# Optimization experiments

Hardware: AMD Instinct MI355X
Metric: run time of the kernel (lower is better)

## Reference

```python
import jax, jax.numpy as jnp
import numpy as np

EPS = 1e-6
HID = 2048; N_HEADS = 16; Q_LORA = 768; KV_LORA = 512
ROPE_D = 64; NOPE_D = 128; V_D = 128
IDX_H = 32; IDX_D = 128; IDX_TOPK = 512
N_EXP = 8; TOPK = 4; N_GROUP = 4; TOPK_GROUP = 2
MOE_I = 512; SHARED_I = 512; ROUTED_SCALE = 2.5
T = 1024
NEG = -1e30


def _rms(x, w, eps=EPS):
    x = x.astype(jnp.float32)
    return x * jax.lax.rsqrt(jnp.mean(x * x, axis=-1, keepdims=True) + eps) * w


def _ln(x, w, b, eps=EPS):
    x = x.astype(jnp.float32)
    m = jnp.mean(x, axis=-1, keepdims=True)
    v = jnp.mean((x - m) ** 2, axis=-1, keepdims=True)
    return (x - m) * jax.lax.rsqrt(v + eps) * w + b


def _rope_cs(positions, dim):
    inv = 1.0 / (10000.0 ** (jnp.arange(0, dim, 2, dtype=jnp.float32) / dim))
    f = positions.astype(jnp.float32)[:, None] * inv[None, :]  # [T, dim/2]
    return jnp.cos(f), jnp.sin(f)


def _rope(x, cos, sin):
    # neox-style rotate-half over last dim
    d = x.shape[-1] // 2
    x1, x2 = x[..., :d], x[..., d:]
    while cos.ndim < x.ndim:
        cos, sin = cos[:, None], sin[:, None]
    return jnp.concatenate([x1 * cos - x2 * sin, x2 * cos + x1 * sin], axis=-1)


def setup_inputs() -> dict:
    key = jax.random.key(0)
    ks = iter(jax.random.split(key, 32))
    w = lambda *s: jax.random.normal(next(ks), s, jnp.float32) * 0.02
    inp = {
        'positions': jnp.arange(T, dtype=jnp.int32),
        'hidden_states': jax.random.normal(next(ks), (T, HID), jnp.float32),
        'residual': jax.random.normal(next(ks), (T, HID), jnp.float32),
        'w_input_ln': jnp.ones((HID,), jnp.float32),
        'w_post_ln': jnp.ones((HID,), jnp.float32),
        'w_step1': w(Q_LORA + KV_LORA + ROPE_D + IDX_D + IDX_H, HID),
        'w_q_a_ln': jnp.ones((Q_LORA,), jnp.float32),
        'w_kv_a_ln': jnp.ones((KV_LORA,), jnp.float32),
        'idx_k_ln_w': jnp.ones((IDX_D,), jnp.float32),
        'idx_k_ln_b': jnp.zeros((IDX_D,), jnp.float32),
        'w_step3': w(IDX_H * IDX_D + N_HEADS * (NOPE_D + ROPE_D), Q_LORA),
        'W_UK_T': w(N_HEADS, NOPE_D, KV_LORA),
        'W_UV': w(N_HEADS, KV_LORA, V_D),
        'w_o': w(HID, N_HEADS * V_D),
        'gate_w': w(N_EXP, HID),
        'gate_bias': jnp.zeros((N_EXP,), jnp.float32),
        'shared_gate_up': w(2 * SHARED_I, HID),
        'shared_down': w(HID, SHARED_I),
        'exp_gate_up': w(N_EXP, 2 * MOE_I, HID),
        'exp_down': w(N_EXP, HID, MOE_I),
    }
    return inp


def reference(positions, hidden_states, residual, w_input_ln, w_post_ln, w_step1,
              w_q_a_ln, w_kv_a_ln, idx_k_ln_w, idx_k_ln_b, w_step3, W_UK_T, W_UV,
              w_o, gate_w, gate_bias, shared_gate_up, shared_down, exp_gate_up, exp_down):
    Tn = hidden_states.shape[0]
    rows = jnp.arange(Tn)
    # (allreduce is identity at tp=1) + residual add + RMSNorm
    res = hidden_states.astype(jnp.float32) + residual.astype(jnp.float32)
    h = _rms(res, w_input_ln)
    # ---- Step 1: fused qkv_a + indexer_wk + indexer_weights_proj GEMM ----
    s1 = h @ w_step1.T
    o0 = 0
    q_c = s1[:, o0:o0 + Q_LORA]; o0 += Q_LORA
    kv_c = s1[:, o0:o0 + KV_LORA]; o0 += KV_LORA
    k_pe = s1[:, o0:o0 + ROPE_D]; o0 += ROPE_D
    idx_k = s1[:, o0:o0 + IDX_D]; o0 += IDX_D
    idx_w_raw = s1[:, o0:o0 + IDX_H]
    cos, sin = _rope_cs(positions, ROPE_D)
    # fused_norm_rope: norms + rope on k_pe / indexer-k
    q_c = _rms(q_c, w_q_a_ln)
    kv_c = _rms(kv_c, w_kv_a_ln)
    k_pe = _rope(k_pe, cos, sin)
    idx_k = _ln(idx_k, idx_k_ln_w, idx_k_ln_b)
    idx_k = jnp.concatenate([_rope(idx_k[:, :ROPE_D], cos, sin), idx_k[:, ROPE_D:]], axis=-1)
    # ---- Step 3: fused indexer_wq_b + q_b_proj GEMM ----
    s3 = q_c @ w_step3.T
    idx_q = s3[:, :IDX_H * IDX_D].reshape(Tn, IDX_H, IDX_D)
    q = s3[:, IDX_H * IDX_D:].reshape(Tn, N_HEADS, NOPE_D + ROPE_D)
    q_nope, q_pe = q[..., :NOPE_D], q[..., NOPE_D:]
    # absorb W_UK: [T,H,nope] x [H,nope,kv_lora] -> [T,H,kv_lora]
    ql_nope = jnp.einsum('thn,hnk->thk', q_nope, W_UK_T)
    q_pe = _rope(q_pe, cos, sin)
    idx_q = jnp.concatenate([_rope(idx_q[..., :ROPE_D], cos, sin), idx_q[..., ROPE_D:]], axis=-1)
    idx_q = idx_q * (IDX_D ** -0.5)            # indexer softmax scale
    idx_w = idx_w_raw * (IDX_H ** -0.5)        # per-head weights scale
    # ---- sparse attention indexer: relu(q.k) head-weighted sum, causal top-k ----
    il = jnp.einsum('thd,sd->ths', idx_q, idx_k)          # [T,Hi,S]
    iscores = jnp.einsum('ths,th->ts', jax.nn.relu(il), idx_w)
    causal = positions[:, None] >= positions[None, :]
    iscores = jnp.where(causal, iscores, NEG)
    topk_idx = jax.lax.top_k(iscores, IDX_TOPK)[1]        # [T, IDX_TOPK]
    tmask = jnp.zeros((Tn, Tn), bool).at[rows[:, None], topk_idx].set(True)
    mask = causal & tmask
    # ---- MLA MQA attention in latent space ----
    mqa_q = jnp.concatenate([ql_nope, jnp.broadcast_to(q_pe, (Tn, N_HEADS, ROPE_D))], axis=-1)
    kv = jnp.concatenate([kv_c, k_pe], axis=-1)           # [S, kv_lora+rope]
    att = jnp.einsum('thd,sd->hts', mqa_q, kv) * ((NOPE_D + ROPE_D) ** -0.5)
    att = jnp.where(mask[None], att, NEG)
    p = jax.nn.softmax(att, axis=-1)
    o = jnp.einsum('hts,sk->thk', p, kv_c)                # [T,H,kv_lora]
    o = jnp.einsum('thk,hkv->thv', o, W_UV).reshape(Tn, N_HEADS * V_D)
    attn_out = o @ w_o.T
    # add + RMSNorm
    res2 = attn_out + res
    h2 = _rms(res2, w_post_ln)
    # ---- MoE: DeepSeekV3 sigmoid grouped routing + shared experts ----
    glog = h2 @ gate_w.T
    sg = jax.nn.sigmoid(glog)
    sc = sg + gate_bias
    gsz = N_EXP // N_GROUP
    grp = sc.reshape(Tn, N_GROUP, gsz)
    grp_score = jax.lax.top_k(grp, min(2, gsz))[0].sum(-1)
    gidx = jax.lax.top_k(grp_score, TOPK_GROUP)[1]
    gmask = jnp.zeros((Tn, N_GROUP), bool).at[rows[:, None], gidx].set(True)
    emask = jnp.repeat(gmask, gsz, axis=1)
    sc_m = jnp.where(emask, sc, NEG)
    _, tid = jax.lax.top_k(sc_m, TOPK)
    tw = jnp.take_along_axis(sg, tid, axis=1)
    tw = tw / (tw.sum(-1, keepdims=True) + 1e-20) * ROUTED_SCALE
    comb = jnp.zeros((Tn, N_EXP), jnp.float32).at[rows[:, None], tid].set(tw)
    # routed experts (dense masked combine as reference for grouped-GEMM dispatch)
    gu = jnp.einsum('th,eih->tei', h2, exp_gate_up)       # [T,E,2I]
    act = jax.nn.silu(gu[..., :MOE_I]) * gu[..., MOE_I:]
    routed_e = jnp.einsum('tei,ehi->teh', act, exp_down)  # [T,E,H]
    routed = jnp.einsum('te,teh->th', comb, routed_e)
    # shared experts
    gus = h2 @ shared_gate_up.T
    shared = (jax.nn.silu(gus[:, :SHARED_I]) * gus[:, SHARED_I:]) @ shared_down.T
    out = shared + routed
    return out, res2
```

## Files before the change

kernel.cpp:

```cpp
#include <hip/hip_runtime.h>
#include <math.h>

static constexpr int TT  = 1024;
static constexpr int HID = 2048;
static constexpr int NH  = 16;
static constexpr int QL  = 768;
static constexpr int KVL = 512;
static constexpr int RD  = 64;
static constexpr int IH  = 32;
static constexpr int ID  = 128;
static constexpr int S1W = QL + KVL + RD + ID + IH;
static constexpr int S3W = IH*ID + NH*(128+RD);

#define SCALE_ATT 0.07216878364870323f
#define SC_IDXQ   0.08838834764831845f
#define SC_IDXW   0.17677669529663687f
#define NEGR      -1e30f
#define NEGL      -3.0e38f

typedef __bf16 bf16x8 __attribute__((ext_vector_type(8)));
typedef float  f32x4  __attribute__((ext_vector_type(4)));

#define GLD_LDS16(g, l) __builtin_amdgcn_global_load_lds( \
    (const __attribute__((address_space(1))) void*)(g),   \
    (__attribute__((address_space(3))) void*)(l), 16, 0, 0)

__device__ __forceinline__ unsigned short f2b(float x) {
  union { float f; unsigned u; } v; v.f = x;
  unsigned r = v.u + 0x7FFFu + ((v.u >> 16) & 1u);
  return (unsigned short)(r >> 16);
}
__device__ __forceinline__ float b2f(unsigned short u) {
  union { unsigned u; float f; } v; v.u = ((unsigned)u) << 16;
  return v.f;
}

__device__ __forceinline__ float blk_sum256(float v, float* s) {
  #pragma unroll
  for (int o = 32; o > 0; o >>= 1) v += __shfl_down(v, o, 64);
  __syncthreads();
  if ((threadIdx.x & 63) == 0) s[threadIdx.x >> 6] = v;
  __syncthreads();
  return s[0] + s[1] + s[2] + s[3];
}

__global__ __launch_bounds__(256) void k_prelude(const float* __restrict__ hs,
                                                 const float* __restrict__ rsd,
                                                 const float* __restrict__ w,
                                                 float* __restrict__ res,
                                                 unsigned short* __restrict__ hb) {
  int t = blockIdx.x;
  __shared__ float scr[4];
  float vals[8]; float ss = 0.f;
  #pragma unroll
  for (int r = 0; r < 8; r++) {
    int d = threadIdx.x + 256*r;
    float v = hs[(size_t)t*HID + d] + rsd[(size_t)t*HID + d];
    vals[r] = v; res[(size_t)t*HID + d] = v; ss = fmaf(v, v, ss);
  }
  ss = blk_sum256(ss, scr);
  float inv = 1.f/sqrtf(ss/(float)HID + 1e-6f);
  #pragma unroll
  for (int r = 0; r < 8; r++) {
    int d = threadIdx.x + 256*r;
    hb[(size_t)t*HID + d] = f2b(vals[r]*inv*w[d]);
  }
}

__global__ __launch_bounds__(256) void k_res2(const float* __restrict__ attn1,
                                              const float* __restrict__ attn2,
                                              const float* __restrict__ res,
                                              const float* __restrict__ w,
                                              float* __restrict__ res2_out,
                                              float* __restrict__ h2,
                                              unsigned short* __restrict__ h2b) {
  int t = blockIdx.x;
  __shared__ float scr[4];
  float vals[8]; float ss = 0.f;
  #pragma unroll
  for (int r = 0; r < 8; r++) {
    int d = threadIdx.x + 256*r;
    float v = attn1[(size_t)t*HID + d] + attn2[(size_t)t*HID + d] + res[(size_t)t*HID + d];
    vals[r] = v; res2_out[(size_t)t*HID + d] = v; ss = fmaf(v, v, ss);
  }
  ss = blk_sum256(ss, scr);
  float inv = 1.f/sqrtf(ss/(float)HID + 1e-6f);
  #pragma unroll
  for (int r = 0; r < 8; r++) {
    int d = threadIdx.x + 256*r;
    float o = vals[r]*inv*w[d];
    h2[(size_t)t*HID + d] = o;
    h2b[(size_t)t*HID + d] = f2b(o);
  }
}

__global__ void k_ropecs(const int* __restrict__ pos, float* __restrict__ cosb, float* __restrict__ sinb) {
  int i = blockIdx.x*256 + threadIdx.x;
  if (i >= TT*32) return;
  int t = i >> 5, k = i & 31;
  double inv = pow(10000.0, -((double)(2*k))/64.0);
  double f = (double)pos[t] * inv;
  cosb[i] = (float)cos(f);
  sinb[i] = (float)sin(f);
}

__global__ void k_f2b(const float* __restrict__ s, unsigned short* __restrict__ d,
                      long long n, long long ntot) {
  long long stride = (long long)gridDim.x * 1024;
  for (long long i = ((long long)blockIdx.x*256 + threadIdx.x)*4; i < ntot; i += stride) {
    float x0, x1, x2, x3;
    if (i + 3 < n) { float4 v = *(const float4*)(s + i); x0=v.x; x1=v.y; x2=v.z; x3=v.w; }
    else {
      x0 = (i   < n) ? s[i]   : 0.f; x1 = (i+1 < n) ? s[i+1] : 0.f;
      x2 = (i+2 < n) ? s[i+2] : 0.f; x3 = (i+3 < n) ? s[i+3] : 0.f;
    }
    ushort4 o; o.x=f2b(x0); o.y=f2b(x1); o.z=f2b(x2); o.w=f2b(x3);
    *(ushort4*)(d + i) = o;
  }
}

__global__ void k_f2b4(const float* __restrict__ s0, unsigned short* __restrict__ d0, long long n0,
                       const float* __restrict__ s1, unsigned short* __restrict__ d1, long long n1,
                       const float* __restrict__ s2, unsigned short* __restrict__ d2, long long n2,
                       const float* __restrict__ s3, unsigned short* __restrict__ d3, long long n3) {
  long long ntot = n0 + n1 + n2 + n3;
  long long stride = (long long)gridDim.x * 1024;
  for (long long i = ((long long)blockIdx.x*256 + threadIdx.x)*4; i < ntot; i += stride) {
    const float* s; unsigned short* d; long long j = i;
    if (j < n0) { s = s0; d = d0; }
    else { j -= n0;
      if (j < n1) { s = s1; d = d1; }
      else { j -= n1;
        if (j < n2) { s = s2; d = d2; }
        else { j -= n2; s = s3; d = d3; } } }
    float4 v = *(const float4*)(s + j);
    ushort4 o; o.x=f2b(v.x); o.y=f2b(v.y); o.z=f2b(v.z); o.w=f2b(v.w);
    *(ushort4*)(d + j) = o;
  }
}

__global__ __launch_bounds__(256) void k_tconvb(const float* __restrict__ src,
                                                unsigned short* __restrict__ dst,
                                                int R, int C) {
  src += (size_t)blockIdx.z * R * C;
  dst += (size_t)blockIdx.z * R * C;
  __shared__ float tile[32][33];
  int c0 = blockIdx.x * 32, r0 = blockIdx.y * 32;
  int tx = threadIdx.x & 31, ty = threadIdx.x >> 5;
  #pragma unroll
  for (int i = 0; i < 4; i++) {
    int r = r0 + ty + i*8;
    tile[ty + i*8][tx] = src[(size_t)r*C + c0 + tx];
  }
  __syncthreads();
  #pragma unroll
  for (int i = 0; i < 4; i++) {
    int c = c0 + ty + i*8;
    dst[(size_t)c*R + r0 + tx] = f2b(tile[tx][ty + i*8]);
  }
}

template<int OUT, bool ILV>
__global__ __launch_bounds__(256) void k_mgemm(
    const unsigned short* __restrict__ A, int lda, long long sA,
    const unsigned short* __restrict__ B, int ldb, long long sB,
    void* __restrict__ Cv, int ldc, long long sC,
    int N, int K, float alpha, int cskip, int ktri,
    int nseg, long long segA, long long segB,
    const float* __restrict__ comb) {
  const int row0 = blockIdx.y * 128;
  const int col0 = blockIdx.x * 128;
  if (cskip >= 0 && col0 > row0 + cskip) return;
  __shared__ __align__(16) unsigned short As[128*64];
  __shared__ __align__(16) unsigned short Bs[128*64];
  const int tid  = threadIdx.x;
  const int wave = tid >> 6, lane = tid & 63;
  const int wm = wave >> 1, wn = wave & 1;
  const int zb = blockIdx.z;
  A += (size_t)zb * (size_t)sA;
  B += (size_t)zb * (size_t)sB;

  f32x4 acc[4][4] = {};
  const int l15 = lane & 15, l4 = lane >> 4;
  const int sx = l15 & 7;
  const int Kend = (ktri && K > row0 + 128) ? (row0 + 128) : K;

  for (int seg = 0; seg < nseg; seg++) {
    const unsigned short* Ab = A + (size_t)seg * segA;
    const unsigned short* Bb = B + (size_t)seg * segB;
    for (int k0 = 0; k0 < Kend; k0 += 64) {
      __syncthreads();
      #pragma unroll
      for (int it = 0; it < 4; it++) {
        int base = wave*64 + it*256;
        int sidx = base + lane;
        int r = sidx >> 3, s = sidx & 7;
        int s_src = s ^ (r & 7);
        const unsigned short* ga = Ab + (size_t)(row0 + r)*lda + k0 + s_src*8;
        GLD_LDS16(ga, As + base*8);
        int rt = col0 + r;
        int srow = ILV ? ((rt >> 1) + (rt & 1)*512) : rt;
        const unsigned short* gb = Bb + (size_t)srow*ldb + k0 + s_src*8;
        GLD_LDS16(gb, Bs + base*8);
      }
      __syncthreads();
      #pragma unroll
      for (int kc = 0; kc < 2; kc++) {
        const int sl = ((kc*4 + l4) ^ sx) << 3;
        bf16x8 fa[4], fb[4];
        #pragma unroll
        for (int mf = 0; mf < 4; mf++)
          fa[mf] = *(const bf16x8*)&As[(wm*64 + mf*16 + l15)*64 + sl];
        #pragma unroll
        for (int nf = 0; nf < 4; nf++)
          fb[nf] = *(const bf16x8*)&Bs[(wn*64 + nf*16 + l15)*64 + sl];
        #pragma unroll
        for (int mf = 0; mf < 4; mf++)
          #pragma unroll
          for (int nf = 0; nf < 4; nf++)
            acc[mf][nf] = __builtin_amdgcn_mfma_f32_16x16x32_bf16(fa[mf], fb[nf], acc[mf][nf], 0, 0, 0);
      }
    }
  }

  #pragma unroll
  for (int mf = 0; mf < 4; mf++) {
    #pragma unroll
    for (int nf = 0; nf < 4; nf++) {
      int n = col0 + wn*64 + nf*16 + l15;
      #pragma unroll
      for (int r = 0; r < 4; r++) {
        int m = row0 + wm*64 + mf*16 + l4*4 + r;
        float v = acc[mf][nf][r] * alpha;
        if (OUT == 2) {
          float p = __shfl_xor(v, 1, 64);
          if ((l15 & 1) == 0) {
            float w = (zb < 8) ? comb[m*8 + zb] : 1.f;
            float rres = v/(1.f + expf(-v)) * p * w;
            ((unsigned short*)Cv)[(size_t)zb*sC + (size_t)m*ldc + (n >> 1)] = f2b(rres);
          }
        } else if (n < N) {
          size_t idx = (size_t)m*ldc + n;
          if (OUT == 1) ((unsigned short*)Cv)[(size_t)zb*sC + idx] = f2b(v);
          else          ((float*)Cv)[(size_t)zb*sC + idx] = v;
        }
      }
    }
  }
}

__global__ __launch_bounds__(256) void k_post1(const float* __restrict__ s1a,
    const float* __restrict__ s1b,
    const float* __restrict__ wq, const float* __restrict__ wkv,
    const float* __restrict__ lnw, const float* __restrict__ lnb,
    const float* __restrict__ cosb, const float* __restrict__ sinb,
    unsigned short* __restrict__ qcb, float* __restrict__ kvc, float* __restrict__ kpe,
    float* __restrict__ idxk, float* __restrict__ idxw) {
  int t = blockIdx.x, tid = threadIdx.x;
  __shared__ float rowb[S1W];
  __shared__ float scr[4];
  __shared__ float yb[128];
  for (int d = tid; d < S1W; d += 256)
    rowb[d] = s1a[(size_t)t*S1W + d] + s1b[(size_t)t*S1W + d];
  __syncthreads();
  float ss = 0.f;
  for (int d = tid; d < QL; d += 256) { float v = rowb[d]; ss = fmaf(v,v,ss); }
  ss = blk_sum256(ss, scr);
  float inv = 1.f/sqrtf(ss/(float)QL + 1e-6f);
  for (int d = tid; d < QL; d += 256) qcb[(size_t)t*QL + d] = f2b(rowb[d]*inv*wq[d]);
  ss = 0.f;
  for (int d = tid; d < KVL; d += 256) { float v = rowb[QL+d]; ss = fmaf(v,v,ss); }
  ss = blk_sum256(ss, scr);
  inv = 1.f/sqrtf(ss/(float)KVL + 1e-6f);
  for (int d = tid; d < KVL; d += 256) kvc[(size_t)t*KVL + d] = rowb[QL+d]*inv*wkv[d];
  float sm = (tid < 128) ? rowb[1344 + tid] : 0.f;
  float tot = blk_sum256(sm, scr);
  float mean = tot / 128.f;
  float vs = 0.f;
  if (tid < 128) { float v = rowb[1344+tid] - mean; vs = v*v; }
  vs = blk_sum256(vs, scr);
  float ivn = 1.f/sqrtf(vs/128.f + 1e-6f);
  if (tid < 128) yb[tid] = (rowb[1344+tid]-mean)*ivn*lnw[tid] + lnb[tid];
  __syncthreads();
  if (tid < 32) {
    float c = cosb[t*32 + tid], s = sinb[t*32 + tid];
    idxk[(size_t)t*ID + tid]      = yb[tid]*c - yb[32+tid]*s;
    idxk[(size_t)t*ID + 32 + tid] = yb[32+tid]*c + yb[tid]*s;
    float x1 = rowb[1280+tid], x2 = rowb[1312+tid];
    kpe[(size_t)t*RD + tid]      = x1*c - x2*s;
    kpe[(size_t)t*RD + 32 + tid] = x2*c + x1*s;
    idxw[(size_t)t*IH + tid] = rowb[1472+tid] * SC_IDXW;
  } else if (tid >= 64 && tid < 128) {
    idxk[(size_t)t*ID + tid] = yb[tid];
  }
}

__global__ __launch_bounds__(256) void k_post3b(const float* __restrict__ s3,
                                                const float* __restrict__ cosb,
                                                const float* __restrict__ sinb,
                                                unsigned short* __restrict__ s3b) {
  int t = blockIdx.x, tid = threadIdx.x;
  const float* row = s3 + (size_t)t*S3W;
  __shared__ float buf[S3W];
  __shared__ float cs[32], sn[32];
  if (tid < 32) { cs[tid] = cosb[t*32+tid]; sn[tid] = sinb[t*32+tid]; }
  for (int d = tid; d < S3W; d += 256) buf[d] = row[d];
  __syncthreads();
  for (int p = tid; p < 1024; p += 256) {
    int h = p >> 5, d = p & 31;
    float c = cs[d], s = sn[d];
    float x1 = buf[h*ID + d], x2 = buf[h*ID + 32 + d];
    buf[h*ID + d]      = (x1*c - x2*s) * SC_IDXQ;
    buf[h*ID + 32 + d] = (x2*c + x1*s) * SC_IDXQ;
  }
  for (int p = tid; p < 2048; p += 256) {
    int h = p >> 6, d = 64 + (p & 63);
    buf[h*ID + d] *= SC_IDXQ;
  }
  for (int p = tid; p < 512; p += 256) {
    int h = p >> 5, d = p & 31;
    float c = cs[d], s = sn[d];
    int base = IH*ID + h*192 + 128;
    float x1 = buf[base + d], x2 = buf[base + 32 + d];
    buf[base + d]      = x1*c - x2*s;
    buf[base + 32 + d] = x2*c + x1*s;
  }
  __syncthreads();
  unsigned short* orow = s3b + (size_t)t*S3W;
  for (int g = tid*4; g < S3W; g += 1024) {
    ushort4 o;
    o.x = f2b(buf[g]); o.y = f2b(buf[g+1]); o.z = f2b(buf[g+2]); o.w = f2b(buf[g+3]);
    *(ushort4*)(orow + g) = o;
  }
}

__global__ void k_qpe(const unsigned short* __restrict__ s3b, unsigned short* __restrict__ qm) {
  int i = blockIdx.x*256 + threadIdx.x;
  int t = i >> 10, r = i & 1023;
  int h = r >> 6, j = r & 63;
  float v = b2f(s3b[(size_t)t*S3W + IH*ID + h*192 + 128 + j]) * SCALE_ATT;
  qm[(size_t)t*9216 + h*576 + 512 + j] = f2b(v);
}

__global__ void k_kvb(const float* __restrict__ kvc, const float* __restrict__ kpe,
                      unsigned short* __restrict__ kvb) {
  int i = blockIdx.x*256 + threadIdx.x;
  int s = i / 576, d = i - s*576;
  float v = (d < 512) ? kvc[(size_t)s*KVL + d] : kpe[(size_t)s*RD + (d - 512)];
  kvb[i] = f2b(v);
}

__global__ __launch_bounds__(256) void k_ired(const float* __restrict__ il,
                                              const float* __restrict__ idxw,
                                              float* __restrict__ isc,
                                              int first, int last, int h0) {
  int tr = blockIdx.x;
  int t = 512 + tr;
  int s0 = threadIdx.x * 4;
  float4 acc;
  if (first) acc = make_float4(0.f, 0.f, 0.f, 0.f);
  else       acc = *(float4*)(isc + (size_t)tr*TT + s0);
  #pragma unroll
  for (int hh = 0; hh < 8; hh++) {
    float w = idxw[t*IH + h0 + hh];
    float4 v = *(const float4*)(il + (size_t)hh*524288 + (size_t)tr*1024 + s0);
    acc.x += fmaxf(v.x, 0.f) * w;
    acc.y += fmaxf(v.y, 0.f) * w;
    acc.z += fmaxf(v.z, 0.f) * w;
    acc.w += fmaxf(v.w, 0.f) * w;
  }
  if (last) {
    if (s0     > t) acc.x = NEGR;
    if (s0 + 1 > t) acc.y = NEGR;
    if (s0 + 2 > t) acc.z = NEGR;
    if (s0 + 3 > t) acc.w = NEGR;
  }
  *(float4*)(isc + (size_t)tr*TT + s0) = acc;
}

__global__ __launch_bounds__(512) void k_topk(const float* __restrict__ isc,
                                              unsigned char* __restrict__ mask) {
  int t = 512 + blockIdx.x;
  const float* row = isc + (size_t)blockIdx.x * TT;
  __shared__ unsigned long long keys[1024];
  int tid = threadIdx.x;
  for (int i = tid; i < 1024; i += 512) {
    float v = row[i];
    unsigned int b = __float_as_uint(v);
    unsigned int u = (b & 0x80000000u) ? ~b : (b | 0x80000000u);
    keys[i] = ((unsigned long long)u << 32) | (unsigned int)(1023 - i);
  }
  __syncthreads();
  for (int k = 2; k <= 1024; k <<= 1) {
    for (int j = k >> 1; j > 0; j >>= 1) {
      int i = ((tid & ~(j - 1)) << 1) | (tid & (j - 1));
      int l = i | j;
      unsigned long long a = keys[i], b = keys[l];
      bool up = ((i & k) == 0);
      if ((a < b) == up) { keys[i] = b; keys[l] = a; }
      __syncthreads();
    }
  }
  unsigned char* mrow = mask + (size_t)t * TT;
  for (int p = tid; p < 1024; p += 512) {
    int s = 1023 - (int)(keys[p] & 0xFFFFFFFFu);
    mrow[s] = (p < 512) ? (unsigned char)1 : (unsigned char)0;
  }
}

__global__ __launch_bounds__(256) void k_psoft(unsigned short* __restrict__ pb,
                                               const unsigned char* __restrict__ mask) {
  int b = blockIdx.x;
  int t = b & 1023, h = b >> 10;
  unsigned short* row = pb + ((size_t)h << 20) + ((size_t)t << 10);
  int tid = threadIdx.x;
  __shared__ float scr[4];
  int s0 = tid * 4;
  int rub = ((t >> 7) + 1) << 7;
  bool act = (s0 < rub);
  float v0 = 0.f, v1 = 0.f, v2 = 0.f, v3 = 0.f;
  bool m0 = false, m1 = false, m2 = false, m3 = false;
  if (act) {
    ushort4 raw = *(const ushort4*)(row + s0);
    v0 = b2f(raw.x); v1 = b2f(raw.y); v2 = b2f(raw.z); v3 = b2f(raw.w);
    if (t < 512) {
      m0 = (s0 <= t); m1 = (s0+1 <= t); m2 = (s0+2 <= t); m3 = (s0+3 <= t);
    } else {
      uchar4 mk = *(const uchar4*)(mask + (size_t)t*TT + s0);
      m0 = (s0 <= t) && mk.x; m1 = (s0+1 <= t) && mk.y;
      m2 = (s0+2 <= t) && mk.z; m3 = (s0+3 <= t) && mk.w;
    }
  }
  float mx = NEGL;
  if (m0) mx = v0;
  if (m1) mx = fmaxf(mx, v1);
  if (m2) mx = fmaxf(mx, v2);
  if (m3) mx = fmaxf(mx, v3);
  #pragma unroll
  for (int o = 32; o > 0; o >>= 1) mx = fmaxf(mx, __shfl_down(mx, o, 64));
  __syncthreads();
  if ((tid & 63) == 0) scr[tid >> 6] = mx;
  __syncthreads();
  mx = fmaxf(fmaxf(scr[0], scr[1]), fmaxf(scr[2], scr[3]));
  float p0 = m0 ? expf(v0 - mx) : 0.f;
  float p1 = m1 ? expf(v1 - mx) : 0.f;
  float p2 = m2 ? expf(v2 - mx) : 0.f;
  float p3 = m3 ? expf(v3 - mx) : 0.f;
  float sum = blk_sum256((p0+p1)+(p2+p3), scr);
  float inv = 1.f / sum;
  if (act) {
    ushort4 o;
    o.x = f2b(p0*inv); o.y = f2b(p1*inv); o.z = f2b(p2*inv); o.w = f2b(p3*inv);
    *(ushort4*)(row + s0) = o;
  }
}

__global__ __launch_bounds__(256) void k_gate(const float* __restrict__ h2,
                                              const float* __restrict__ gw,
                                              const float* __restrict__ gb,
                                              float* __restrict__ comb) {
  int t = blockIdx.x, tid = threadIdx.x;
  int e = tid >> 5, lane = tid & 31;
  __shared__ float gl[8];
  float p = 0.f;
  for (int d = lane; d < HID; d += 32) p = fmaf(h2[(size_t)t*HID+d], gw[(size_t)e*HID+d], p);
  #pragma unroll
  for (int o = 16; o > 0; o >>= 1) p += __shfl_down(p, o, 32);
  if (lane == 0) gl[e] = p;
  __syncthreads();
  if (tid == 0) {
    float sg[8], sc[8];
    #pragma unroll
    for (int i = 0; i < 8; i++) { sg[i] = 1.f/(1.f+expf(-gl[i])); sc[i] = sg[i] + gb[i]; }
    float gs[4];
    #pragma unroll
    for (int g = 0; g < 4; g++) gs[g] = sc[2*g] + sc[2*g+1];
    int g0 = 0;
    for (int g = 1; g < 4; g++) if (gs[g] > gs[g0]) g0 = g;
    int g1 = -1;
    for (int g = 0; g < 4; g++) { if (g == g0) continue; if (g1 < 0 || gs[g] > gs[g1]) g1 = g; }
    float wsum = 1e-20f;
    #pragma unroll
    for (int i = 0; i < 8; i++) { int g = i >> 1; if (g == g0 || g == g1) wsum += sg[i]; }
    #pragma unroll
    for (int i = 0; i < 8; i++) { int g = i >> 1; comb[t*8+i] = (g == g0 || g == g1) ? sg[i]/wsum*2.5f : 0.f; }
  }
}

__global__ void k_dnred(const float* __restrict__ r, float* __restrict__ o) {
  int i = (blockIdx.x*256 + threadIdx.x)*4;
  float4 a = *(const float4*)(r + i);
  float4 b = *(const float4*)(r + 2097152 + i);
  float4 c = *(const float4*)(r + 4194304 + i);
  float4 v;
  v.x = a.x + b.x + c.x; v.y = a.y + b.y + c.y;
  v.z = a.z + b.z + c.z; v.w = a.w + b.w + c.w;
  *(float4*)(o + i) = v;
}

extern "C" void kernel_launch(void* const* d_in, const int* in_sizes, int n_in,
                              void* d_out, int out_size, void* d_ws, size_t ws_size,
                              hipStream_t stream) {
  const int*   positions = (const int*)d_in[0];
  const float* hs     = (const float*)d_in[1];
  const float* rsd    = (const float*)d_in[2];
  const float* w_in   = (const float*)d_in[3];
  const float* w_post = (const float*)d_in[4];
  const float* w_s1   = (const float*)d_in[5];
  const float* w_qln  = (const float*)d_in[6];
  const float* w_kvln = (const float*)d_in[7];
  const float* iklnw  = (const float*)d_in[8];
  const float* iklnb  = (const float*)d_in[9];
  const float* w_s3   = (const float*)d_in[10];
  const float* wukt   = (const float*)d_in[11];
  const float* wuv    = (const float*)d_in[12];
  const float* w_o    = (const float*)d_in[13];
  const float* gate_w = (const float*)d_in[14];
  const float* gate_b = (const float*)d_in[15];
  const float* sh_gu  = (const float*)d_in[16];
  const float* sh_dn  = (const float*)d_in[17];
  const float* ex_gu  = (const float*)d_in[18];
  const float* ex_dn  = (const float*)d_in[19];

  float* ws = (float*)d_ws;
  typedef unsigned short ush;
  float* RES   = ws + 0;
  float* COSB  = ws + 2097152;
  float* SINB  = ws + 2129920;
  float* KVC   = ws + 2162688;
  float* KPE   = ws + 2686976;
  float* IDXK  = ws + 2752512;
  float* IDXW  = ws + 2883584;
  float* COMB  = ws + 2916352;
  ush*   HB    = (ush*)(ws + 2924544);
  ush*   WS1B  = (ush*)(ws + 3973120);
  float* S1P0  = ws + 5545984;
  ush*   QCB   = (ush*)(ws + 7086080);
  ush*   WS3B  = (ush*)(ws + 7479296);
  ush*   WOB   = (ush*)(ws + 7479296);
  float* S3    = ws + 10231808;
  float* S1P1  = ws + 10231808;
  ush*   S3B   = (ush*)(ws + 17571840);
  ush*   WUKTB = (ush*)(ws + 21241856);
  ush*   QMQAB = (ush*)(ws + 21766144);
  float* ISC   = ws + 26484736;
  unsigned char* MASK = (unsigned char*)(ws + 27009024);
  ush*   WUVB  = (ush*)(ws + 27271168);
  ush*   KVB   = (ush*)(ws + 27795456);
  ush*   VTB   = (ush*)(ws + 28090368);
  ush*   O2B   = (ush*)(ws + 28352512);
  float* ILB   = ws + 27795456;
  ush*   IDXKB = (ush*)(ws + 31989760);
  ush*   PB    = (ush*)(ws + 10231808);
  ush*   OHB   = (ush*)(ws + 18620416);
  float* ATTNP = ws + 10231808;
  float* H2     = ws + 2924544;
  ush*   H2B    = (ush*)(ws + 5021696);
  ush*   EXGUB  = (ush*)(ws + 6070272);
  ush*   SHGUB  = (ush*)(ws + 14458880);
  ush*   EXDNB  = (ush*)(ws + 15507456);
  ush*   SHDNB  = (ush*)(ws + 19701760);
  ush*   ACTB9  = (ush*)(ws + 20226048);
  float* RPART  = ws + 22585344;

  float* OUT0 = (float*)d_out;
  float* OUT_RES2 = OUT0 + (size_t)TT*HID;

  k_prelude<<<TT, 256, 0, stream>>>(hs, rsd, w_in, RES, HB);
  k_ropecs<<<(TT*32)/256, 256, 0, stream>>>(positions, COSB, SINB);
  k_f2b<<<1024, 256, 0, stream>>>(w_s1, WS1B, 3080192LL, 3145728LL);
  k_f2b<<<1024, 256, 0, stream>>>(w_s3, WS3B, 5505024LL, 5505024LL);
  k_tconvb<<<dim3(16,4,16), 256, 0, stream>>>(wukt, WUKTB, 128, 512);
  k_tconvb<<<dim3(4,16,16), 256, 0, stream>>>(wuv, WUVB, 512, 128);
  k_mgemm<0,false><<<dim3(12,8,2), 256, 0, stream>>>(
      HB, 2048, 1024, WS1B, 2048, 1024, S1P0, S1W, 4685824,
      1504, 1024, 1.f, -1, 0, 1, 0, 0, nullptr);
  k_post1<<<TT, 256, 0, stream>>>(S1P0, S1P1, w_qln, w_kvln, iklnw, iklnb, COSB, SINB, QCB, KVC, KPE, IDXK, IDXW);
  k_f2b<<<128, 256, 0, stream>>>(IDXK, IDXKB, 131072LL, 131072LL);
  k_mgemm<0,false><<<dim3(56,8,1), 256, 0, stream>>>(
      QCB, 768, 0, WS3B, 768, 0, S3, S3W, 0,
      S3W, 768, 1.f, -1, 0, 1, 0, 0, nullptr);
  k_post3b<<<TT, 256, 0, stream>>>(S3, COSB, SINB, (ush*)S3B);
  k_f2b<<<1024, 256, 0, stream>>>(w_o, WOB, 4194304LL, 4194304LL);
  k_mgemm<1,false><<<dim3(4,8,16), 256, 0, stream>>>(
      S3B + 4096, S3W, 192, WUKTB, 128, 65536, QMQAB, 9216, 576,
      512, 128, SCALE_ATT, -1, 0, 1, 0, 0, nullptr);
  k_qpe<<<4096, 256, 0, stream>>>(S3B, QMQAB);
  for (int c = 0; c < 4; c++) {
    k_mgemm<0,false><<<dim3(8,4,8), 256, 0, stream>>>(
        S3B + (size_t)512*S3W + c*1024, S3W, 128, IDXKB, 128, 0,
        ILB, 1024, 524288, 1024, 128, 1.f, 639, 0, 1, 0, 0, nullptr);
    k_ired<<<512, 256, 0, stream>>>(ILB, IDXW, ISC, c == 0, c == 3, c*8);
  }
  k_topk<<<512, 512, 0, stream>>>(ISC, MASK);
  k_kvb<<<2304, 256, 0, stream>>>(KVC, KPE, KVB);
  k_tconvb<<<dim3(16,32,1), 256, 0, stream>>>(KVC, VTB, 1024, 512);
  k_mgemm<1,false><<<dim3(8,8,16), 256, 0, stream>>>(
      QMQAB, 9216, 576, KVB, 576, 0, PB, 1024, 1048576,
      1024, 576, 1.f, 127, 0, 1, 0, 0, nullptr);
  k_psoft<<<16384, 256, 0, stream>>>(PB, MASK);
  k_mgemm<1,false><<<dim3(4,8,16), 256, 0, stream>>>(
      PB, 1024, 1048576, VTB, 1024, 0, OHB, 512, 524288,
      512, 1024, 1.f, -1, 1, 1, 0, 0, nullptr);
  k_mgemm<1,false><<<dim3(1,8,16), 256, 0, stream>>>(
      OHB, 512, 524288, WUVB, 512, 65536, O2B, 2048, 128,
      128, 512, 1.f, -1, 0, 1, 0, 0, nullptr);
  k_mgemm<0,false><<<dim3(16,8,2), 256, 0, stream>>>(
      O2B, 2048, 1024, WOB, 2048, 1024, ATTNP, 2048, 2097152,
      2048, 1024, 1.f, -1, 0, 1, 0, 0, nullptr);
  k_res2<<<TT, 256, 0, stream>>>(ATTNP, ATTNP + 2097152, RES, w_post, OUT_RES2, H2, H2B);
  k_gate<<<TT, 256, 0, stream>>>(H2, gate_w, gate_b, COMB);
  k_f2b4<<<2048, 256, 0, stream>>>(ex_gu, EXGUB, 16777216LL,
                                   sh_gu, SHGUB, 2097152LL,
                                   ex_dn, EXDNB, 8388608LL,
                                   sh_dn, SHDNB, 1048576LL);
  k_mgemm<2,true><<<dim3(8,8,9), 256, 0, stream>>>(
      H2B, 2048, 0, EXGUB, 2048, 2097152, ACTB9, 512, 524288,
      1024, 2048, 1.f, -1, 0, 1, 0, 0, COMB);
  k_mgemm<0,false><<<dim3(16,8,3), 256, 0, stream>>>(
      ACTB9, 512, 1572864, EXDNB, 512, 3145728, RPART, 2048, 2097152,
      2048, 512, 1.f, -1, 0, 3, 524288, 1048576, nullptr);
  k_dnred<<<2048, 256, 0, stream>>>(RPART, OUT0);
}
```

Before: 443.7 us.

## Replace dense masked MoE with routed grouped-GEMM token dispatch

```diff
diff --git a/kernel.cpp b/kernel.cpp
--- a/kernel.cpp
+++ b/kernel.cpp
@@ -160,25 +160,42 @@
   }
 }
 
-template<int OUT, bool ILV>
+template<int OUT, bool ILV, int MOE>
 __global__ __launch_bounds__(256) void k_mgemm(
     const unsigned short* __restrict__ A, int lda, long long sA,
     const unsigned short* __restrict__ B, int ldb, long long sB,
     void* __restrict__ Cv, int ldc, long long sC,
     int N, int K, float alpha, int cskip, int ktri,
     int nseg, long long segA, long long segB,
-    const float* __restrict__ comb) {
+    const float* __restrict__ comb,
+    const int* __restrict__ cntp, const int* __restrict__ tokp) {
   const int row0 = blockIdx.y * 128;
   const int col0 = blockIdx.x * 128;
   if (cskip >= 0 && col0 > row0 + cskip) return;
+  const int zb = blockIdx.z;
+  int cnt = 0; long long off = 0;
+  if (MOE) {
+    cnt = cntp[zb];
+    for (int e = 0; e < zb; e++) off += cntp[e];
+    if (row0 >= cnt) return;
+  }
   __shared__ __align__(16) unsigned short As[128*64];
   __shared__ __align__(16) unsigned short Bs[128*64];
   const int tid  = threadIdx.x;
   const int wave = tid >> 6, lane = tid & 63;
   const int wm = wave >> 1, wn = wave & 1;
-  const int zb = blockIdx.z;
   A += (size_t)zb * (size_t)sA;
   B += (size_t)zb * (size_t)sB;
+  if (MOE == 2) A += off * (long long)lda;
+
+  int tki[4];
+  if (MOE == 1) {
+    #pragma unroll
+    for (int it = 0; it < 4; it++) {
+      int r = (wave*64 + it*256 + lane) >> 3;
+      tki[it] = tokp[zb*1024 + row0 + r];
+    }
+  }
 
   f32x4 acc[4][4] = {};
   const int l15 = lane & 15, l4 = lane >> 4;
@@ -196,7 +213,9 @@
         int sidx = base + lane;
         int r = sidx >> 3, s = sidx & 7;
         int s_src = s ^ (r & 7);
-        const unsigned short* ga = Ab + (size_t)(row0 + r)*lda + k0 + s_src*8;
+        const unsigned short* ga;
+        if (MOE == 1) ga = Ab + (size_t)tki[it]*lda + k0 + s_src*8;
+        else          ga = Ab + (size_t)(row0 + r)*lda + k0 + s_src*8;
         GLD_LDS16(ga, As + base*8);
         int rt = col0 + r;
         int srow = ILV ? ((rt >> 1) + (rt & 1)*512) : rt;
@@ -235,14 +254,30 @@
         if (OUT == 2) {
           float p = __shfl_xor(v, 1, 64);
           if ((l15 & 1) == 0) {
-            float w = (zb < 8) ? comb[m*8 + zb] : 1.f;
-            float rres = v/(1.f + expf(-v)) * p * w;
-            ((unsigned short*)Cv)[(size_t)zb*sC + (size_t)m*ldc + (n >> 1)] = f2b(rres);
+            bool ok = true;
+            long long mrow = m;
+            float w;
+            if (MOE == 1) {
+              ok = (m < cnt); mrow = off + m;
+              int tok = tokp[zb*1024 + m];
+              w = (zb < 8) ? comb[tok*8 + zb] : 1.f;
+            } else {
+              w = (zb < 8) ? comb[m*8 + zb] : 1.f;
+            }
+            if (ok) {
+              float rres = v/(1.f + expf(-v)) * p * w;
+              ((unsigned short*)Cv)[(size_t)zb*sC + (size_t)mrow*ldc + (n >> 1)] = f2b(rres);
+            }
           }
         } else if (n < N) {
-          size_t idx = (size_t)m*ldc + n;
-          if (OUT == 1) ((unsigned short*)Cv)[(size_t)zb*sC + idx] = f2b(v);
-          else          ((float*)Cv)[(size_t)zb*sC + idx] = v;
+          bool ok = true;
+          long long mrow = m;
+          if (MOE == 2) { ok = (m < cnt); mrow = off + m; }
+          if (ok) {
+            size_t idx = (size_t)mrow*ldc + n;
+            if (OUT == 1) ((unsigned short*)Cv)[(size_t)zb*sC + idx] = f2b(v);
+            else          ((float*)Cv)[(size_t)zb*sC + idx] = v;
+          }
         }
       }
     }
@@ -487,15 +522,62 @@
   }
 }
 
-__global__ void k_dnred(const float* __restrict__ r, float* __restrict__ o) {
-  int i = (blockIdx.x*256 + threadIdx.x)*4;
-  float4 a = *(const float4*)(r + i);
-  float4 b = *(const float4*)(r + 2097152 + i);
-  float4 c = *(const float4*)(r + 4194304 + i);
-  float4 v;
-  v.x = a.x + b.x + c.x; v.y = a.y + b.y + c.y;
-  v.z = a.z + b.z + c.z; v.w = a.w + b.w + c.w;
-  *(float4*)(o + i) = v;
+__global__ __launch_bounds__(1024) void k_route(const float* __restrict__ comb,
+                                                int* __restrict__ tokidx,
+                                                int* __restrict__ rank,
+                                                int* __restrict__ cntp) {
+  int e = blockIdx.x;
+  int t = threadIdx.x;
+  if (e == 8) {
+    tokidx[8*1024 + t] = t;
+    if (t == 0) cntp[8] = 1024;
+    return;
+  }
+  int lane = t & 63, w = t >> 6;
+  bool sel = comb[t*8 + e] != 0.0f;
+  unsigned long long bal = __ballot(sel);
+  int pw = __popcll(bal & ((1ull << lane) - 1ull));
+  int wt = __popcll(bal);
+  __shared__ int wsum[16];
+  if (lane == 0) wsum[w] = wt;
+  __syncthreads();
+  int woff = 0, total = 0;
+  #pragma unroll
+  for (int i = 0; i < 16; i++) { int v = wsum[i]; if (i < w) woff += v; total += v; }
+  int pos = woff + pw;
+  rank[t*8 + e] = sel ? pos : -1;
+  if (sel) tokidx[e*1024 + pos] = t;
+  __syncthreads();
+  if (t >= total) tokidx[e*1024 + t] = 0;
+  if (t == 0) cntp[e] = total;
+}
+
+__global__ __launch_bounds__(256) void k_rsum(const float* __restrict__ dpc,
+                                              const int* __restrict__ rank,
+                                              const int* __restrict__ cntp,
+                                              float* __restrict__ out) {
+  int t = blockIdx.x;
+  int d = threadIdx.x * 8;
+  int offs[8]; int acc_off = 0;
+  #pragma unroll
+  for (int e = 0; e < 8; e++) { offs[e] = acc_off; acc_off += cntp[e]; }
+  const float* ps = dpc + (size_t)(acc_off + t)*2048 + d;
+  float4 a0 = *(const float4*)ps;
+  float4 a1 = *(const float4*)(ps + 4);
+  #pragma unroll
+  for (int e = 0; e < 8; e++) {
+    int r = rank[t*8 + e];
+    if (r >= 0) {
+      const float* p = dpc + (size_t)(offs[e] + r)*2048 + d;
+      float4 b0 = *(const float4*)p;
+      float4 b1 = *(const float4*)(p + 4);
+      a0.x += b0.x; a0.y += b0.y; a0.z += b0.z; a0.w += b0.w;
+      a1.x += b1.x; a1.y += b1.y; a1.z += b1.z; a1.w += b1.w;
+    }
+  }
+  float* po = out + (size_t)t*2048 + d;
+  *(float4*)po = a0;
+  *(float4*)(po + 4) = a1;
 }
 
 extern "C" void kernel_launch(void* const* d_in, const int* in_sizes, int n_in,
@@ -560,8 +642,11 @@
   ush*   SHGUB  = (ush*)(ws + 14458880);
   ush*   EXDNB  = (ush*)(ws + 15507456);
   ush*   SHDNB  = (ush*)(ws + 19701760);
-  ush*   ACTB9  = (ush*)(ws + 20226048);
-  float* RPART  = ws + 22585344;
+  ush*   ACTC   = (ush*)(ws + 20226048);
+  float* DPC    = ws + 21536768;
+  int*   TOKIDX = (int*)(ws + 32022528);
+  int*   RANK   = (int*)(ws + 32031744);
+  int*   CNT    = (int*)(ws + 32039936);
 
   float* OUT0 = (float*)d_out;
   float* OUT_RES2 = OUT0 + (size_t)TT*HID;
@@ -572,53 +657,54 @@
   k_f2b<<<1024, 256, 0, stream>>>(w_s3, WS3B, 5505024LL, 5505024LL);
   k_tconvb<<<dim3(16,4,16), 256, 0, stream>>>(wukt, WUKTB, 128, 512);
   k_tconvb<<<dim3(4,16,16), 256, 0, stream>>>(wuv, WUVB, 512, 128);
-  k_mgemm<0,false><<<dim3(12,8,2), 256, 0, stream>>>(
+  k_mgemm<0,false,0><<<dim3(12,8,2), 256, 0, stream>>>(
       HB, 2048, 1024, WS1B, 2048, 1024, S1P0, S1W, 4685824,
-      1504, 1024, 1.f, -1, 0, 1, 0, 0, nullptr);
+      1504, 1024, 1.f, -1, 0, 1, 0, 0, nullptr, nullptr, nullptr);
   k_post1<<<TT, 256, 0, stream>>>(S1P0, S1P1, w_qln, w_kvln, iklnw, iklnb, COSB, SINB, QCB, KVC, KPE, IDXK, IDXW);
   k_f2b<<<128, 256, 0, stream>>>(IDXK, IDXKB, 131072LL, 131072LL);
-  k_mgemm<0,false><<<dim3(56,8,1), 256, 0, stream>>>(
+  k_mgemm<0,false,0><<<dim3(56,8,1), 256, 0, stream>>>(
       QCB, 768, 0, WS3B, 768, 0, S3, S3W, 0,
-      S3W, 768, 1.f, -1, 0, 1, 0, 0, nullptr);
+      S3W, 768, 1.f, -1, 0, 1, 0, 0, nullptr, nullptr, nullptr);
   k_post3b<<<TT, 256, 0, stream>>>(S3, COSB, SINB, (ush*)S3B);
   k_f2b<<<1024, 256, 0, stream>>>(w_o, WOB, 4194304LL, 4194304LL);
-  k_mgemm<1,false><<<dim3(4,8,16), 256, 0, stream>>>(
+  k_mgemm<1,false,0><<<dim3(4,8,16), 256, 0, stream>>>(
       S3B + 4096, S3W, 192, WUKTB, 128, 65536, QMQAB, 9216, 576,
-      512, 128, SCALE_ATT, -1, 0, 1, 0, 0, nullptr);
+      512, 128, SCALE_ATT, -1, 0, 1, 0, 0, nullptr, nullptr, nullptr);
   k_qpe<<<4096, 256, 0, stream>>>(S3B, QMQAB);
   for (int c = 0; c < 4; c++) {
-    k_mgemm<0,false><<<dim3(8,4,8), 256, 0, stream>>>(
+    k_mgemm<0,false,0><<<dim3(8,4,8), 256, 0, stream>>>(
         S3B + (size_t)512*S3W + c*1024, S3W, 128, IDXKB, 128, 0,
-        ILB, 1024, 524288, 1024, 128, 1.f, 639, 0, 1, 0, 0, nullptr);
+        ILB, 1024, 524288, 1024, 128, 1.f, 639, 0, 1, 0, 0, nullptr, nullptr, nullptr);
     k_ired<<<512, 256, 0, stream>>>(ILB, IDXW, ISC, c == 0, c == 3, c*8);
   }
   k_topk<<<512, 512, 0, stream>>>(ISC, MASK);
   k_kvb<<<2304, 256, 0, stream>>>(KVC, KPE, KVB);
   k_tconvb<<<dim3(16,32,1), 256, 0, stream>>>(KVC, VTB, 1024, 512);
-  k_mgemm<1,false><<<dim3(8,8,16), 256, 0, stream>>>(
+  k_mgemm<1,false,0><<<dim3(8,8,16), 256, 0, stream>>>(
       QMQAB, 9216, 576, KVB, 576, 0, PB, 1024, 1048576,
-      1024, 576, 1.f, 127, 0, 1, 0, 0, nullptr);
+      1024, 576, 1.f, 127, 0, 1, 0, 0, nullptr, nullptr, nullptr);
   k_psoft<<<16384, 256, 0, stream>>>(PB, MASK);
-  k_mgemm<1,false><<<dim3(4,8,16), 256, 0, stream>>>(
+  k_mgemm<1,false,0><<<dim3(4,8,16), 256, 0, stream>>>(
       PB, 1024, 1048576, VTB, 1024, 0, OHB, 512, 524288,
-      512, 1024, 1.f, -1, 1, 1, 0, 0, nullptr);
-  k_mgemm<1,false><<<dim3(1,8,16), 256, 0, stream>>>(
+      512, 1024, 1.f, -1, 1, 1, 0, 0, nullptr, nullptr, nullptr);
+  k_mgemm<1,false,0><<<dim3(1,8,16), 256, 0, stream>>>(
       OHB, 512, 524288, WUVB, 512, 65536, O2B, 2048, 128,
-      128, 512, 1.f, -1, 0, 1, 0, 0, nullptr);
-  k_mgemm<0,false><<<dim3(16,8,2), 256, 0, stream>>>(
+      128, 512, 1.f, -1, 0, 1, 0, 0, nullptr, nullptr, nullptr);
+  k_mgemm<0,false,0><<<dim3(16,8,2), 256, 0, stream>>>(
       O2B, 2048, 1024, WOB, 2048, 1024, ATTNP, 2048, 2097152,
-      2048, 1024, 1.f, -1, 0, 1, 0, 0, nullptr);
+      2048, 1024, 1.f, -1, 0, 1, 0, 0, nullptr, nullptr, nullptr);
   k_res2<<<TT, 256, 0, stream>>>(ATTNP, ATTNP + 2097152, RES, w_post, OUT_RES2, H2, H2B);
   k_gate<<<TT, 256, 0, stream>>>(H2, gate_w, gate_b, COMB);
+  k_route<<<9, 1024, 0, stream>>>(COMB, TOKIDX, RANK, CNT);
   k_f2b4<<<2048, 256, 0, stream>>>(ex_gu, EXGUB, 16777216LL,
                                    sh_gu, SHGUB, 2097152LL,
                                    ex_dn, EXDNB, 8388608LL,
                                    sh_dn, SHDNB, 1048576LL);
-  k_mgemm<2,true><<<dim3(8,8,9), 256, 0, stream>>>(
-      H2B, 2048, 0, EXGUB, 2048, 2097152, ACTB9, 512, 524288,
-      1024, 2048, 1.f, -1, 0, 1, 0, 0, COMB);
-  k_mgemm<0,false><<<dim3(16,8,3), 256, 0, stream>>>(
-      ACTB9, 512, 1572864, EXDNB, 512, 3145728, RPART, 2048, 2097152,
-      2048, 512, 1.f, -1, 0, 3, 524288, 1048576, nullptr);
-  k_dnred<<<2048, 256, 0, stream>>>(RPART, OUT0);
-}
+  k_mgemm<2,true,1><<<dim3(8,8,9), 256, 0, stream>>>(
+      H2B, 2048, 0, EXGUB, 2048, 2097152, ACTC, 512, 0,
+      1024, 2048, 1.f, -1, 0, 1, 0, 0, COMB, CNT, TOKIDX);
+  k_mgemm<0,false,2><<<dim3(16,8,9), 256, 0, stream>>>(
+      ACTC, 512, 0, EXDNB, 512, 1048576, DPC, 2048, 0,
+      2048, 512, 1.f, -1, 0, 1, 0, 0, nullptr, CNT, nullptr);
+  k_rsum<<<TT, 256, 0, stream>>>(DPC, RANK, CNT, OUT0);
+}
```

Result: slower. 454.0 us (+2.3%).
